# Kernel optimization log

Measured on AMD Instinct MI355X. Metric: run time of the kernel, lower is better.

## Reference

```python
import jax, jax.numpy as jnp
import numpy as np

EPS = 1e-5

def _bn(x, g, b, m, v):
    # eval-mode BatchNorm over channel dim (x: [N, C])
    return (x - m) * jax.lax.rsqrt(v + EPS) * g + b

def setup_inputs() -> dict:
    key = jax.random.key(0)
    ks = jax.random.split(key, 12)
    B, T, C, H, W = 16, 8, 512, 28, 28
    c8 = C // 8
    inp = {}
    inp['x'] = jax.random.normal(ks[0], (B * T, C, H, W), jnp.float32)
    inp['w1'] = jax.random.normal(ks[1], (c8, C), jnp.float32) * 0.05
    inp['bn1_g'] = jnp.ones((c8,), jnp.float32)
    inp['bn1_b'] = jnp.zeros((c8,), jnp.float32)
    inp['bn1_m'] = jax.random.normal(ks[2], (c8,), jnp.float32) * 0.1
    inp['bn1_v'] = jax.random.uniform(ks[3], (c8,), jnp.float32) + 0.5
    inp['w2'] = jax.random.normal(ks[4], (c8, C), jnp.float32) * 0.05
    inp['bn2_g'] = jnp.ones((c8,), jnp.float32)
    inp['bn2_b'] = jnp.zeros((c8,), jnp.float32)
    inp['bn2_m'] = jax.random.normal(ks[5], (c8,), jnp.float32) * 0.1
    inp['bn2_v'] = jax.random.uniform(ks[6], (c8,), jnp.float32) + 0.5
    inp['Wa_w'] = jax.random.normal(ks[7], (C, c8), jnp.float32) * 0.05
    inp['Wa_b'] = jnp.zeros((C,), jnp.float32)
    inp['gamma_w'] = jax.random.normal(ks[8], (2 * c8,), jnp.float32) * 0.05
    inp['gamma_b'] = jnp.zeros((1,), jnp.float32)
    inp['n_segment'] = T
    return inp

def reference(x, w1, bn1_g, bn1_b, bn1_m, bn1_v, w2, bn2_g, bn2_b, bn2_m, bn2_v, Wa_w, Wa_b, gamma_w, gamma_b, n_segment):
    nt, c, h, w = x.shape
    T = n_segment
    B = nt // T
    # adaptive_avg_pool2d to 1x1 == spatial mean -> [nt, c]
    xv = jnp.mean(x, axis=(2, 3))
    # 1x1 conv on 1x1 spatial map == channel matmul; conv -> BN -> ReLU
    left = jax.nn.relu(_bn(xv @ w1.T, bn1_g, bn1_b, bn1_m, bn1_v)).reshape(B, T, -1)
    right = jax.nn.relu(_bn(xv @ w2.T, bn2_g, bn2_b, bn2_m, bn2_v)).reshape(B, T, -1)
    # temporal difference, pad last step with constant 1 (matches F.pad value=1)
    diff = jnp.concatenate(
        [left[:, :-1] - right[:, 1:], jnp.ones((B, 1, left.shape[-1]), x.dtype)], axis=1)

    def step(g_state, d_t):
        # g_state, d_t: [B, c//8]
        cat = jnp.concatenate([d_t, g_state], axis=1)            # [B, c//4]
        g = jax.nn.sigmoid(cat @ gamma_w + gamma_b[0])[:, None]  # [B, 1] gate
        new = d_t * g + g_state * (1.0 - g)
        att = jax.nn.sigmoid(new @ Wa_w.T + Wa_b)                # [B, c]
        return new, att

    # initial x_global = x_vec_diff[:, -1] (the padded ones slice)
    _, atts = jax.lax.scan(step, diff[:, -1], jnp.swapaxes(diff, 0, 1))
    sig = jnp.swapaxes(atts, 0, 1)                               # [B, T, c]
    out = x.reshape(B, T, c, h, w) * sig[:, :, :, None, None]
    return out.reshape(nt, c, h, w)
```

## Files before the change

kernel.cpp:

```cpp
#include <hip/hip_runtime.h>
#include <hip/hip_bf16.h>
#include <math.h>

constexpr int NT  = 128;
constexpr int C   = 512;
constexpr int HW  = 784;
constexpr int C8  = 64;
constexpr int TT  = 8;
constexpr int BB  = 16;
constexpr float EPS = 1e-5f;

__global__ void k_mean(const float* __restrict__ x, float* __restrict__ xv) {
    const int wave = threadIdx.x >> 6;
    const int lane = threadIdx.x & 63;
    const size_t row = (size_t)blockIdx.x * 4 + wave;
    const float4* p = (const float4*)(x + row * HW);
    float s = 0.f;
    #pragma unroll
    for (int j = lane; j < HW / 4; j += 64) {
        float4 v = p[j];
        s += v.x + v.y + v.z + v.w;
    }
    #pragma unroll
    for (int off = 32; off; off >>= 1) s += __shfl_xor(s, off);
    if (lane == 0) xv[row] = s * (1.0f / HW);
}

__global__ void k_lr(const float* __restrict__ xv,
                     const float* __restrict__ w1,
                     const float* __restrict__ g1, const float* __restrict__ b1,
                     const float* __restrict__ m1, const float* __restrict__ v1,
                     const float* __restrict__ w2,
                     const float* __restrict__ g2, const float* __restrict__ b2,
                     const float* __restrict__ m2, const float* __restrict__ v2,
                     float* __restrict__ lr) {
    __shared__ float sx[C];
    const int bt = blockIdx.x;
    for (int i = threadIdx.x; i < C; i += 256) sx[i] = xv[bt * C + i];
    __syncthreads();

    const int out  = threadIdx.x >> 1;
    const int half = threadIdx.x & 1;
    const int j    = out & 63;
    const float* w = (out < C8) ? (w1 + (size_t)j * C) : (w2 + (size_t)j * C);
    const int k0 = half * (C / 2);
    float acc = 0.f;
    #pragma unroll 8
    for (int k = 0; k < C / 2; ++k) acc = fmaf(sx[k0 + k], w[k0 + k], acc);
    acc += __shfl_xor(acc, 1);
    if (half == 0) {
        float y;
        if (out < C8) y = (acc - m1[j]) * rsqrtf(v1[j] + EPS) * g1[j] + b1[j];
        else          y = (acc - m2[j]) * rsqrtf(v2[j] + EPS) * g2[j] + b2[j];
        lr[bt * 2 * C8 + out] = fmaxf(y, 0.f);
    }
}

__global__ void k_scan(const float* __restrict__ lr,
                       const float* __restrict__ gamma_w,
                       const float* __restrict__ gamma_b,
                       float* __restrict__ Nw) {
    const int b = blockIdx.x;
    const int j = threadIdx.x;
    const float gw0 = gamma_w[j];
    const float gw1 = gamma_w[C8 + j];
    const float gb  = gamma_b[0];

    float d[TT];
    #pragma unroll
    for (int t = 0; t < TT - 1; ++t)
        d[t] = lr[(b * TT + t) * (2 * C8) + j]
             - lr[(b * TT + t + 1) * (2 * C8) + C8 + j];
    d[TT - 1] = 1.0f;

    float state = 1.0f;
    #pragma unroll
    for (int t = 0; t < TT; ++t) {
        float part = d[t] * gw0 + state * gw1;
        #pragma unroll
        for (int off = 32; off; off >>= 1) part += __shfl_xor(part, off);
        const float g = 1.f / (1.f + expf(-(part + gb)));
        state = d[t] * g + state * (1.f - g);
        Nw[(b * TT + t) * C8 + j] = state;
    }
}

__global__ void k_att(const float* __restrict__ Nw,
                      const float* __restrict__ Wa_w,
                      const float* __restrict__ Wa_b,
                      float* __restrict__ sig) {
    __shared__ float sn[C8];
    const int bt = blockIdx.x;
    if (threadIdx.x < C8) sn[threadIdx.x] = Nw[bt * C8 + threadIdx.x];
    __syncthreads();
    for (int c = threadIdx.x; c < C; c += 256) {
        const float* w = Wa_w + (size_t)c * C8;
        float acc = Wa_b[c];
        #pragma unroll 16
        for (int k = 0; k < C8; ++k) acc = fmaf(sn[k], w[k], acc);
        sig[bt * C + c] = 1.f / (1.f + expf(-acc));
    }
}

__global__ void k_scale(const float* __restrict__ x,
                        const float* __restrict__ sig,
                        float* __restrict__ out) {
    const int wave = threadIdx.x >> 6;
    const int lane = threadIdx.x & 63;
    const size_t row = (size_t)blockIdx.x * 4 + wave;
    const float s = sig[row];
    const float4* px = (const float4*)(x + row * HW);
    float4*       po = (float4*)(out + row * HW);
    #pragma unroll
    for (int j = lane; j < HW / 4; j += 64) {
        float4 v = px[j];
        v.x *= s; v.y *= s; v.z *= s; v.w *= s;
        po[j] = v;
    }
}

extern "C" void kernel_launch(void* const* d_in, const int* in_sizes, int n_in,
                              void* d_out, int out_size, void* d_ws, size_t ws_size,
                              hipStream_t stream) {
    const float* x     = (const float*)d_in[0];
    const float* w1    = (const float*)d_in[1];
    const float* bn1_g = (const float*)d_in[2];
    const float* bn1_b = (const float*)d_in[3];
    const float* bn1_m = (const float*)d_in[4];
    const float* bn1_v = (const float*)d_in[5];
    const float* w2    = (const float*)d_in[6];
    const float* bn2_g = (const float*)d_in[7];
    const float* bn2_b = (const float*)d_in[8];
    const float* bn2_m = (const float*)d_in[9];
    const float* bn2_v = (const float*)d_in[10];
    const float* Wa_w  = (const float*)d_in[11];
    const float* Wa_b  = (const float*)d_in[12];
    const float* gamma_w = (const float*)d_in[13];
    const float* gamma_b = (const float*)d_in[14];
    float* out = (float*)d_out;

    float* ws  = (float*)d_ws;
    float* xv  = ws;
    float* lr  = xv + NT * C;
    float* Nw  = lr + NT * 2 * C8;
    float* sig = Nw + NT * C8;

    const int rows = NT * C;
    k_mean <<<rows / 4, 256, 0, stream>>>(x, xv);
    k_lr   <<<NT, 256, 0, stream>>>(xv, w1, bn1_g, bn1_b, bn1_m, bn1_v,
                                        w2, bn2_g, bn2_b, bn2_m, bn2_v, lr);
    k_scan <<<BB, 64, 0, stream>>>(lr, gamma_w, gamma_b, Nw);
    k_att  <<<NT, 256, 0, stream>>>(Nw, Wa_w, Wa_b, sig);
    k_scale<<<rows / 4, 256, 0, stream>>>(x, sig, out);
}
```

Measured before the change: 420.5 us.

## Process two rows per wave, vectorize small matvecs, use nontemporal stores

The mean and scale kernels now handle two rows per wave so more loads are in flight, and the launch grids are halved to match. The scale kernel writes its output with nontemporal stores to avoid polluting the cache. The two small matvec kernels (left/right projection and attention) are rewritten to use float4 coalesced weight loads with wave-level shuffle reductions instead of per-thread strided dot products. Main time is still in the two bandwidth-bound passes over x, so gains depend on memory-level parallelism and store behaviour.

```diff
diff --git a/kernel.cpp b/kernel.cpp
--- a/kernel.cpp
+++ b/kernel.cpp
@@ -10,20 +10,30 @@
 constexpr int BB  = 16;
 constexpr float EPS = 1e-5f;
 
+typedef float v4f __attribute__((ext_vector_type(4)));
+
 __global__ void k_mean(const float* __restrict__ x, float* __restrict__ xv) {
     const int wave = threadIdx.x >> 6;
     const int lane = threadIdx.x & 63;
-    const size_t row = (size_t)blockIdx.x * 4 + wave;
-    const float4* p = (const float4*)(x + row * HW);
-    float s = 0.f;
-    #pragma unroll
+    const size_t r0 = ((size_t)blockIdx.x * 4 + wave) * 2;
+    const float4* p0 = (const float4*)(x + r0 * HW);
+    const float4* p1 = (const float4*)(x + (r0 + 1) * HW);
+    float s0 = 0.f, s1 = 0.f;
     for (int j = lane; j < HW / 4; j += 64) {
-        float4 v = p[j];
-        s += v.x + v.y + v.z + v.w;
-    }
-    #pragma unroll
-    for (int off = 32; off; off >>= 1) s += __shfl_xor(s, off);
-    if (lane == 0) xv[row] = s * (1.0f / HW);
+        float4 a = p0[j];
+        float4 b = p1[j];
+        s0 += a.x + a.y + a.z + a.w;
+        s1 += b.x + b.y + b.z + b.w;
+    }
+    #pragma unroll
+    for (int off = 32; off; off >>= 1) {
+        s0 += __shfl_xor(s0, off);
+        s1 += __shfl_xor(s1, off);
+    }
+    if (lane == 0) {
+        xv[r0]     = s0 * (1.0f / HW);
+        xv[r0 + 1] = s1 * (1.0f / HW);
+    }
 }
 
 __global__ void k_lr(const float* __restrict__ xv,
@@ -34,25 +44,44 @@
                      const float* __restrict__ g2, const float* __restrict__ b2,
                      const float* __restrict__ m2, const float* __restrict__ v2,
                      float* __restrict__ lr) {
-    __shared__ float sx[C];
-    const int bt = blockIdx.x;
-    for (int i = threadIdx.x; i < C; i += 256) sx[i] = xv[bt * C + i];
-    __syncthreads();
-
-    const int out  = threadIdx.x >> 1;
-    const int half = threadIdx.x & 1;
-    const int j    = out & 63;
-    const float* w = (out < C8) ? (w1 + (size_t)j * C) : (w2 + (size_t)j * C);
-    const int k0 = half * (C / 2);
-    float acc = 0.f;
-    #pragma unroll 8
-    for (int k = 0; k < C / 2; ++k) acc = fmaf(sx[k0 + k], w[k0 + k], acc);
-    acc += __shfl_xor(acc, 1);
-    if (half == 0) {
-        float y;
-        if (out < C8) y = (acc - m1[j]) * rsqrtf(v1[j] + EPS) * g1[j] + b1[j];
-        else          y = (acc - m2[j]) * rsqrtf(v2[j] + EPS) * g2[j] + b2[j];
-        lr[bt * 2 * C8 + out] = fmaxf(y, 0.f);
+    const int bt   = blockIdx.x >> 1;
+    const int side = blockIdx.x & 1;
+    const int wave = threadIdx.x >> 6;
+    const int lane = threadIdx.x & 63;
+
+    const float* wb = side ? w2 : w1;
+    const float* gg = side ? g2 : g1;
+    const float* bb = side ? b2 : b1;
+    const float* mm = side ? m2 : m1;
+    const float* vv = side ? v2 : v1;
+
+    const float4* xr = (const float4*)(xv + (size_t)bt * C);
+    const float4 x0 = xr[lane * 2];
+    const float4 x1 = xr[lane * 2 + 1];
+
+    const int j0 = wave * 16;
+    #pragma unroll
+    for (int jj = 0; jj < 16; jj += 2) {
+        const int ja = j0 + jj, jb2 = j0 + jj + 1;
+        const float4* wa = (const float4*)(wb + (size_t)ja * C);
+        const float4* wc = (const float4*)(wb + (size_t)jb2 * C);
+        float4 a0 = wa[lane * 2], a1 = wa[lane * 2 + 1];
+        float4 c0 = wc[lane * 2], c1 = wc[lane * 2 + 1];
+        float sa = a0.x * x0.x + a0.y * x0.y + a0.z * x0.z + a0.w * x0.w
+                 + a1.x * x1.x + a1.y * x1.y + a1.z * x1.z + a1.w * x1.w;
+        float sc = c0.x * x0.x + c0.y * x0.y + c0.z * x0.z + c0.w * x0.w
+                 + c1.x * x1.x + c1.y * x1.y + c1.z * x1.z + c1.w * x1.w;
+        #pragma unroll
+        for (int off = 32; off; off >>= 1) {
+            sa += __shfl_xor(sa, off);
+            sc += __shfl_xor(sc, off);
+        }
+        if (lane == 0) {
+            float ya = (sa - mm[ja])  * rsqrtf(vv[ja]  + EPS) * gg[ja]  + bb[ja];
+            float yc = (sc - mm[jb2]) * rsqrtf(vv[jb2] + EPS) * gg[jb2] + bb[jb2];
+            lr[bt * 2 * C8 + side * C8 + ja]  = fmaxf(ya, 0.f);
+            lr[bt * 2 * C8 + side * C8 + jb2] = fmaxf(yc, 0.f);
+        }
     }
 }
 
@@ -89,16 +118,28 @@
                       const float* __restrict__ Wa_w,
                       const float* __restrict__ Wa_b,
                       float* __restrict__ sig) {
-    __shared__ float sn[C8];
-    const int bt = blockIdx.x;
-    if (threadIdx.x < C8) sn[threadIdx.x] = Nw[bt * C8 + threadIdx.x];
-    __syncthreads();
-    for (int c = threadIdx.x; c < C; c += 256) {
-        const float* w = Wa_w + (size_t)c * C8;
-        float acc = Wa_b[c];
-        #pragma unroll 16
-        for (int k = 0; k < C8; ++k) acc = fmaf(sn[k], w[k], acc);
-        sig[bt * C + c] = 1.f / (1.f + expf(-acc));
+    const int bt   = blockIdx.x;
+    const int wave = threadIdx.x >> 6;
+    const int lane = threadIdx.x & 63;
+    const int g    = lane >> 3;
+    const int k8   = lane & 7;
+
+    const float4* nr = (const float4*)(Nw + (size_t)bt * C8);
+    const float4 n0 = nr[k8 * 2];
+    const float4 n1 = nr[k8 * 2 + 1];
+
+    #pragma unroll
+    for (int it = 0; it < 16; ++it) {
+        const int c = wave * 128 + it * 8 + g;
+        const float4* wr = (const float4*)(Wa_w + (size_t)c * C8);
+        float4 w0 = wr[k8 * 2], w1 = wr[k8 * 2 + 1];
+        float acc = w0.x * n0.x + w0.y * n0.y + w0.z * n0.z + w0.w * n0.w
+                  + w1.x * n1.x + w1.y * n1.y + w1.z * n1.z + w1.w * n1.w;
+        acc += __shfl_xor(acc, 1);
+        acc += __shfl_xor(acc, 2);
+        acc += __shfl_xor(acc, 4);
+        if (k8 == 0)
+            sig[(size_t)bt * C + c] = 1.f / (1.f + expf(-(acc + Wa_b[c])));
     }
 }
 
@@ -107,15 +148,20 @@
                         float* __restrict__ out) {
     const int wave = threadIdx.x >> 6;
     const int lane = threadIdx.x & 63;
-    const size_t row = (size_t)blockIdx.x * 4 + wave;
-    const float s = sig[row];
-    const float4* px = (const float4*)(x + row * HW);
-    float4*       po = (float4*)(out + row * HW);
-    #pragma unroll
+    const size_t r0 = ((size_t)blockIdx.x * 4 + wave) * 2;
+    const float s0 = sig[r0];
+    const float s1 = sig[r0 + 1];
+    const float4* p0 = (const float4*)(x + r0 * HW);
+    const float4* p1 = (const float4*)(x + (r0 + 1) * HW);
+    v4f* o0 = (v4f*)(out + r0 * HW);
+    v4f* o1 = (v4f*)(out + (r0 + 1) * HW);
     for (int j = lane; j < HW / 4; j += 64) {
-        float4 v = px[j];
-        v.x *= s; v.y *= s; v.z *= s; v.w *= s;
-        po[j] = v;
+        float4 a = p0[j];
+        float4 b = p1[j];
+        v4f av = {a.x * s0, a.y * s0, a.z * s0, a.w * s0};
+        v4f bv = {b.x * s1, b.y * s1, b.z * s1, b.w * s1};
+        __builtin_nontemporal_store(av, o0 + j);
+        __builtin_nontemporal_store(bv, o1 + j);
     }
 }
 
@@ -146,10 +192,10 @@
     float* sig = Nw + NT * C8;
 
     const int rows = NT * C;
-    k_mean <<<rows / 4, 256, 0, stream>>>(x, xv);
-    k_lr   <<<NT, 256, 0, stream>>>(xv, w1, bn1_g, bn1_b, bn1_m, bn1_v,
-                                        w2, bn2_g, bn2_b, bn2_m, bn2_v, lr);
+    k_mean <<<rows / 8, 256, 0, stream>>>(x, xv);
+    k_lr   <<<NT * 2, 256, 0, stream>>>(xv, w1, bn1_g, bn1_b, bn1_m, bn1_v,
+                                            w2, bn2_g, bn2_b, bn2_m, bn2_v, lr);
     k_scan <<<BB, 64, 0, stream>>>(lr, gamma_w, gamma_b, Nw);
     k_att  <<<NT, 256, 0, stream>>>(Nw, Wa_w, Wa_b, sig);
-    k_scale<<<rows / 4, 256, 0, stream>>>(x, sig, out);
-}
+    k_scale<<<rows / 8, 256, 0, stream>>>(x, sig, out);
+}
```

Result: no change. 421.1 us (+0.1%).
